# Kernel optimization log

Hardware: AMD Instinct MI355X
Metric: run time of the kernel (lower is better)

Reference implementation:

```python
import jax, jax.numpy as jnp
import numpy as np

N, D = 8192, 128
NOISEVAR = 1.0

def _softplusinverse(v):
    return np.log(1.0 - np.exp(-v)) + v

def setup_inputs() -> dict:
    key = jax.random.key(0)
    kx, kn = jax.random.split(key)
    x = jax.random.normal(kx, (N, D), dtype=jnp.float32)
    noise = jax.random.normal(kn, (N, D), dtype=jnp.float32)
    phi = jnp.asarray(_softplusinverse(NOISEVAR), dtype=jnp.float32)
    return {"x": x, "phi": phi, "noise": noise}

def reference(x, phi, noise):
    # x: [n, d] encoded features; phi: scalar noise param; noise: [n, d] i.i.d. N(0,1)
    n = x.shape[0]
    var = jax.nn.softplus(phi)
    # Pairwise squared L2 distances via Gram-matrix trick (same math as
    # norm(x_i - x_j)^2, avoids the [n, n, d] broadcast intermediate).
    sq = jnp.sum(x * x, axis=1)                                  # [n]
    d2 = jnp.maximum(sq[:, None] + sq[None, :] - 2.0 * (x @ x.T), 0.0)  # [n, n]
    kde_contribution = jnp.mean(jax.nn.logsumexp(-0.5 * d2 / var, axis=1))
    IXT_nats = jnp.log(jnp.float32(n)) - kde_contribution
    IXT = IXT_nats / jnp.log(jnp.float32(2.0))  # bits=True -> nats2bits
    out = x + var * noise                        # training=True noise injection
    return out, IXT
```

## Files before the change

### kernel.cpp

```cpp
#include <hip/hip_runtime.h>
#include <hip/hip_bf16.h>

#define N 8192
#define D 128
#define TILE 128
#define NT (N / TILE)

typedef __attribute__((ext_vector_type(8))) short short8;
typedef __attribute__((ext_vector_type(4))) float floatx4;
typedef unsigned int u32;

#define GLOAD_LDS16(g, l) \
    __builtin_amdgcn_global_load_lds((const __attribute__((address_space(1))) u32*)(g), \
                                     (__attribute__((address_space(3))) u32*)(l), 16, 0, 0)

static __device__ inline float softplus_of(const float* __restrict__ phi) {
    float p = phi[0];
    return (p > 20.f) ? p : log1pf(__expf(p));
}

static __device__ inline unsigned short f2bf(float f) {
    return __builtin_bit_cast(unsigned short, __float2bfloat16(f));
}

static __device__ inline short8 pack8(float4 a, float4 b) {
    short8 r;
    r[0] = (short)f2bf(a.x); r[1] = (short)f2bf(a.y);
    r[2] = (short)f2bf(a.z); r[3] = (short)f2bf(a.w);
    r[4] = (short)f2bf(b.x); r[5] = (short)f2bf(b.y);
    r[6] = (short)f2bf(b.z); r[7] = (short)f2bf(b.w);
    return r;
}

__global__ __launch_bounds__(256) void k1_cvt(
        const float* __restrict__ x, unsigned short* __restrict__ bf16x,
        float* __restrict__ sq, float* __restrict__ rowsum) {
    int gid = blockIdx.x * 256 + threadIdx.x;
    int row = gid >> 4;
    int gc  = gid & 15;
    const float* src = x + (size_t)row * D + gc * 8;
    float4 u = *(const float4*)src;
    float4 v = *(const float4*)(src + 4);
    short8 p = pack8(u, v);
    int gp = gc ^ (row & 15);
    *(short8*)&bf16x[(size_t)row * D + gp * 8] = p;

    float s = 0.f;
    #pragma unroll
    for (int k = 0; k < 8; k++) {
        u32 bits = ((u32)(unsigned short)p[k]) << 16;
        float b = __builtin_bit_cast(float, bits);
        s += b * b;
    }
    #pragma unroll
    for (int m = 1; m < 16; m <<= 1) s += __shfl_xor(s, m, 64);
    if (gc == 0) { sq[row] = s; rowsum[row] = 0.f; }
}

__global__ __launch_bounds__(256, 2) void k2_gram(
        const unsigned short* __restrict__ bf16x, const float* __restrict__ phi,
        const float* __restrict__ sq, float* __restrict__ rowsum) {
    __shared__ __align__(16) unsigned short Bs[2][TILE * D];

    const int t = threadIdx.x;
    const int wave = t >> 6;
    const int lane = t & 63;
    const int lrow = lane & 15;
    const int quad = lane >> 4;
    const int wr = (wave & 1) * 64;
    const int wc = (wave >> 1) * 64;

    const int b = blockIdx.x;
    const int cnt   = (b < 32) ? 5 : 4;
    const int start = (b < 32) ? 5 * b : 160 + 4 * (b - 32);

    int pti = 0, rem = start, len = NT;
    while (rem >= len) { rem -= len; ++pti; --len; }
    int ptj = pti + rem;

    float var = softplus_of(phi);
    const float e2c = (-0.5f / var) * 1.4426950408889634f;
    const float m2c = -2.0f * e2c;

    {
        const unsigned short* src = bf16x + (size_t)ptj * TILE * D;
        #pragma unroll
        for (int s = 0; s < 8; s++) {
            int cb = s * 256 + wave * 64;
            GLOAD_LDS16(src + (size_t)(cb + lane) * 8, &Bs[0][cb * 8]);
        }
    }
    __syncthreads();

    short8 af[4][4];
    float sie[4][4];
    float rowAcc[4][4];
    int curTi = -1;

    auto flushRow = [&]() {
        const int iBase = curTi * TILE;
        #pragma unroll
        for (int mt = 0; mt < 4; mt++)
            #pragma unroll
            for (int reg = 0; reg < 4; reg++) {
                float v = rowAcc[mt][reg];
                #pragma unroll
                for (int m = 1; m < 16; m <<= 1) v += __shfl_xor(v, m, 64);
                if (lrow == 0)
                    atomicAdd(&rowsum[iBase + wr + mt * 16 + quad * 4 + reg], v);
            }
    };

    for (int r = 0; r < cnt; ++r) {
        const int jBase = ptj * TILE;

        float sje[4];
        #pragma unroll
        for (int nt = 0; nt < 4; nt++)
            sje[nt] = sq[jBase + wc + nt * 16 + lrow] * e2c;

        int nti = pti, ntj = ptj + 1;
        if (ntj == NT) { ++nti; ntj = nti; }
        if (r + 1 < cnt) {
            const unsigned short* src = bf16x + (size_t)ntj * TILE * D;
            unsigned short* dstb = Bs[(r + 1) & 1];
            #pragma unroll
            for (int s = 0; s < 8; s++) {
                int cb = s * 256 + wave * 64;
                GLOAD_LDS16(src + (size_t)(cb + lane) * 8, &dstb[cb * 8]);
            }
        }

        if (pti != curTi) {
            if (curTi >= 0) flushRow();
            const int iBase = pti * TILE;
            #pragma unroll
            for (int mt = 0; mt < 4; mt++) {
                const unsigned short* arow =
                    bf16x + (size_t)(iBase + wr + mt * 16 + lrow) * D;
                #pragma unroll
                for (int kk = 0; kk < 4; kk++)
                    af[mt][kk] = *(const short8*)&arow[((kk * 4 + quad) ^ lrow) * 8];
            }
            #pragma unroll
            for (int mt = 0; mt < 4; mt++)
                #pragma unroll
                for (int reg = 0; reg < 4; reg++) {
                    sie[mt][reg] = sq[iBase + wr + mt * 16 + quad * 4 + reg] * e2c;
                    rowAcc[mt][reg] = 0.f;
                }
            curTi = pti;
        }

        const unsigned short* B = Bs[r & 1];
        floatx4 acc[4][4] = {};
        #pragma unroll
        for (int kk = 0; kk < 4; kk++) {
            short8 bfr[4];
            #pragma unroll
            for (int nt = 0; nt < 4; nt++) {
                int R = wc + nt * 16 + lrow;
                bfr[nt] = *(const short8*)&B[(size_t)R * D + ((kk * 4 + quad) ^ lrow) * 8];
            }
            #pragma unroll
            for (int mt = 0; mt < 4; mt++)
                #pragma unroll
                for (int nt = 0; nt < 4; nt++)
                    acc[mt][nt] = __builtin_amdgcn_mfma_f32_16x16x32_bf16(
                        af[mt][kk], bfr[nt], acc[mt][nt], 0, 0, 0);
        }

        float colAcc[4] = {0.f, 0.f, 0.f, 0.f};
        #pragma unroll
        for (int mt = 0; mt < 4; mt++) {
            #pragma unroll
            for (int reg = 0; reg < 4; reg++) {
                float base = sie[mt][reg];
                #pragma unroll
                for (int nt = 0; nt < 4; nt++) {
                    float p2 = fminf(fmaf(acc[mt][nt][reg], m2c, base + sje[nt]), 0.f);
                    float p = exp2f(p2);
                    rowAcc[mt][reg] += p;
                    colAcc[nt] += p;
                }
            }
        }

        if (pti != ptj) {
            #pragma unroll
            for (int nt = 0; nt < 4; nt++) {
                float v = colAcc[nt];
                v += __shfl_xor(v, 16, 64);
                v += __shfl_xor(v, 32, 64);
                if (quad == 0)
                    atomicAdd(&rowsum[jBase + wc + nt * 16 + lrow], v);
            }
        }

        pti = nti; ptj = ntj;
        __syncthreads();
    }

    flushRow();
}

__global__ __launch_bounds__(1024) void k3_final(
        const float* __restrict__ rowsum, float* __restrict__ out_ixt) {
    __shared__ float red[16];
    int t = threadIdx.x;
    float local = 0.f;
    for (int i = t; i < N; i += 1024) local += logf(rowsum[i]);
    #pragma unroll
    for (int m = 1; m < 64; m <<= 1) local += __shfl_xor(local, m, 64);
    if ((t & 63) == 0) red[t >> 6] = local;
    __syncthreads();
    if (t < 16) {
        float v = red[t];
        #pragma unroll
        for (int m = 1; m < 16; m <<= 1) v += __shfl_xor(v, m, 64);
        if (t == 0) {
            float kde = v / (float)N;
            out_ixt[0] = (logf((float)N) - kde) * 1.4426950408889634f;
        }
    }
}

__global__ __launch_bounds__(256) void k4_noise(
        const float4* __restrict__ x, const float* __restrict__ phi,
        const float4* __restrict__ noise, float4* __restrict__ out) {
    int i = blockIdx.x * 256 + threadIdx.x;
    float var = softplus_of(phi);
    float4 xv = x[i], nv = noise[i];
    float4 ov;
    ov.x = xv.x + var * nv.x;
    ov.y = xv.y + var * nv.y;
    ov.z = xv.z + var * nv.z;
    ov.w = xv.w + var * nv.w;
    out[i] = ov;
}

extern "C" void kernel_launch(void* const* d_in, const int* in_sizes, int n_in,
                              void* d_out, int out_size, void* d_ws, size_t ws_size,
                              hipStream_t stream) {
    const float* x     = (const float*)d_in[0];
    const float* phi   = (const float*)d_in[1];
    const float* noise = (const float*)d_in[2];
    float* out = (float*)d_out;

    float* rowsum = (float*)d_ws;
    float* sq     = rowsum + N;
    unsigned short* bf16x = (unsigned short*)d_out;

    k1_cvt<<<(N * 16) / 256, 256, 0, stream>>>(x, bf16x, sq, rowsum);
    k2_gram<<<512, 256, 0, stream>>>(bf16x, phi, sq, rowsum);
    k3_final<<<1, 1024, 0, stream>>>(rowsum, out + (size_t)N * D);
    k4_noise<<<(N * D / 4) / 256, 256, 0, stream>>>(
        (const float4*)x, phi, (const float4*)noise, (float4*)out);
}
```

Measured before the change: 97.11 us.

## Use per-wave 64x64 tiles with register-resident B and fuse noise output into prep

The Gram kernel now gives each wave its own 64x64 tile pair in the upper-triangular schedule. B fragments are loaded straight from global memory into registers and prefetched for the next tile, replacing the shared-memory double buffer and block-wide barriers. The noise-injection kernel is folded into the conversion kernel, and the bf16 copy moves to workspace so that kernel can write the output directly. This removes LDS traffic, syncs and one launch, but each wave now reloads its B tile from global/L2 with no sharing across the block, and more atomics are issued per output row.

```diff
diff --git a/kernel.cpp b/kernel.cpp
--- a/kernel.cpp
+++ b/kernel.cpp
@@ -3,16 +3,13 @@
 
 #define N 8192
 #define D 128
-#define TILE 128
-#define NT (N / TILE)
+#define T64 64
+#define NT64 (N / T64)
+#define NPAIR (NT64 * (NT64 + 1) / 2)
 
 typedef __attribute__((ext_vector_type(8))) short short8;
 typedef __attribute__((ext_vector_type(4))) float floatx4;
 typedef unsigned int u32;
-
-#define GLOAD_LDS16(g, l) \
-    __builtin_amdgcn_global_load_lds((const __attribute__((address_space(1))) u32*)(g), \
-                                     (__attribute__((address_space(3))) u32*)(l), 16, 0, 0)
 
 static __device__ inline float softplus_of(const float* __restrict__ phi) {
     float p = phi[0];
@@ -32,18 +29,31 @@
     return r;
 }
 
-__global__ __launch_bounds__(256) void k1_cvt(
-        const float* __restrict__ x, unsigned short* __restrict__ bf16x,
-        float* __restrict__ sq, float* __restrict__ rowsum) {
+__global__ __launch_bounds__(256) void k1_prep(
+        const float* __restrict__ x, const float* __restrict__ phi,
+        const float* __restrict__ noise, float* __restrict__ out,
+        unsigned short* __restrict__ bf16x, float* __restrict__ sq,
+        float* __restrict__ rowsum) {
     int gid = blockIdx.x * 256 + threadIdx.x;
     int row = gid >> 4;
     int gc  = gid & 15;
-    const float* src = x + (size_t)row * D + gc * 8;
-    float4 u = *(const float4*)src;
-    float4 v = *(const float4*)(src + 4);
+    float var = softplus_of(phi);
+
+    const float* xs = x     + (size_t)row * D + gc * 8;
+    const float* ns = noise + (size_t)row * D + gc * 8;
+    float4 u  = *(const float4*)xs, v  = *(const float4*)(xs + 4);
+    float4 nu = *(const float4*)ns, nv = *(const float4*)(ns + 4);
+
+    float4 o0, o1;
+    o0.x = u.x + var * nu.x; o0.y = u.y + var * nu.y;
+    o0.z = u.z + var * nu.z; o0.w = u.w + var * nu.w;
+    o1.x = v.x + var * nv.x; o1.y = v.y + var * nv.y;
+    o1.z = v.z + var * nv.z; o1.w = v.w + var * nv.w;
+    float* od = out + (size_t)row * D + gc * 8;
+    *(float4*)od = o0; *(float4*)(od + 4) = o1;
+
     short8 p = pack8(u, v);
-    int gp = gc ^ (row & 15);
-    *(short8*)&bf16x[(size_t)row * D + gp * 8] = p;
+    *(short8*)&bf16x[(size_t)row * D + (size_t)(gc ^ (row & 15)) * 8] = p;
 
     float s = 0.f;
     #pragma unroll
@@ -60,148 +70,139 @@
 __global__ __launch_bounds__(256, 2) void k2_gram(
         const unsigned short* __restrict__ bf16x, const float* __restrict__ phi,
         const float* __restrict__ sq, float* __restrict__ rowsum) {
-    __shared__ __align__(16) unsigned short Bs[2][TILE * D];
-
-    const int t = threadIdx.x;
-    const int wave = t >> 6;
-    const int lane = t & 63;
+    const int w    = blockIdx.x * 4 + (threadIdx.x >> 6);
+    const int lane = threadIdx.x & 63;
     const int lrow = lane & 15;
     const int quad = lane >> 4;
-    const int wr = (wave & 1) * 64;
-    const int wc = (wave >> 1) * 64;
-
-    const int b = blockIdx.x;
-    const int cnt   = (b < 32) ? 5 : 4;
-    const int start = (b < 32) ? 5 * b : 160 + 4 * (b - 32);
-
-    int pti = 0, rem = start, len = NT;
-    while (rem >= len) { rem -= len; ++pti; --len; }
-    int ptj = pti + rem;
+
+    const int cnt = (w < 64) ? 5 : 4;
+    int start     = (w < 64) ? 5 * w : 4 * w + 64;
+    int ti = 0, rem = start, len = NT64;
+    while (rem >= len) { rem -= len; ++ti; --len; }
+    int tj = ti + rem;
 
     float var = softplus_of(phi);
     const float e2c = (-0.5f / var) * 1.4426950408889634f;
     const float m2c = -2.0f * e2c;
 
+    short8 af[4][4], bf[4][4];
+    float  sie[4][4], rowAcc[4][4];
+    int curTi = -1;
+
     {
-        const unsigned short* src = bf16x + (size_t)ptj * TILE * D;
-        #pragma unroll
-        for (int s = 0; s < 8; s++) {
-            int cb = s * 256 + wave * 64;
-            GLOAD_LDS16(src + (size_t)(cb + lane) * 8, &Bs[0][cb * 8]);
-        }
-    }
-    __syncthreads();
-
-    short8 af[4][4];
-    float sie[4][4];
-    float rowAcc[4][4];
-    int curTi = -1;
-
-    auto flushRow = [&]() {
-        const int iBase = curTi * TILE;
-        #pragma unroll
-        for (int mt = 0; mt < 4; mt++)
-            #pragma unroll
-            for (int reg = 0; reg < 4; reg++) {
-                float v = rowAcc[mt][reg];
-                #pragma unroll
-                for (int m = 1; m < 16; m <<= 1) v += __shfl_xor(v, m, 64);
-                if (lrow == 0)
-                    atomicAdd(&rowsum[iBase + wr + mt * 16 + quad * 4 + reg], v);
-            }
-    };
+        const unsigned short* bb = bf16x + (size_t)tj * T64 * D;
+        #pragma unroll
+        for (int nt = 0; nt < 4; nt++) {
+            const unsigned short* br = bb + (size_t)(nt * 16 + lrow) * D;
+            #pragma unroll
+            for (int kk = 0; kk < 4; kk++)
+                bf[nt][kk] = *(const short8*)&br[((kk * 4 + quad) ^ lrow) * 8];
+        }
+    }
 
     for (int r = 0; r < cnt; ++r) {
-        const int jBase = ptj * TILE;
+        const int iB = ti * T64, jB = tj * T64;
 
         float sje[4];
         #pragma unroll
         for (int nt = 0; nt < 4; nt++)
-            sje[nt] = sq[jBase + wc + nt * 16 + lrow] * e2c;
-
-        int nti = pti, ntj = ptj + 1;
-        if (ntj == NT) { ++nti; ntj = nti; }
-        if (r + 1 < cnt) {
-            const unsigned short* src = bf16x + (size_t)ntj * TILE * D;
-            unsigned short* dstb = Bs[(r + 1) & 1];
-            #pragma unroll
-            for (int s = 0; s < 8; s++) {
-                int cb = s * 256 + wave * 64;
-                GLOAD_LDS16(src + (size_t)(cb + lane) * 8, &dstb[cb * 8]);
-            }
-        }
-
-        if (pti != curTi) {
-            if (curTi >= 0) flushRow();
-            const int iBase = pti * TILE;
+            sje[nt] = sq[jB + nt * 16 + lrow] * e2c;
+
+        if (ti != curTi) {
+            if (curTi >= 0) {
+                const int pB = curTi * T64;
+                #pragma unroll
+                for (int mt = 0; mt < 4; mt++)
+                    #pragma unroll
+                    for (int reg = 0; reg < 4; reg++) {
+                        float vv = rowAcc[mt][reg];
+                        #pragma unroll
+                        for (int m = 1; m < 16; m <<= 1) vv += __shfl_xor(vv, m, 64);
+                        if (lrow == 0)
+                            atomicAdd(&rowsum[pB + mt * 16 + quad * 4 + reg], vv);
+                    }
+            }
             #pragma unroll
             for (int mt = 0; mt < 4; mt++) {
-                const unsigned short* arow =
-                    bf16x + (size_t)(iBase + wr + mt * 16 + lrow) * D;
+                const unsigned short* ar = bf16x + (size_t)(iB + mt * 16 + lrow) * D;
                 #pragma unroll
                 for (int kk = 0; kk < 4; kk++)
-                    af[mt][kk] = *(const short8*)&arow[((kk * 4 + quad) ^ lrow) * 8];
+                    af[mt][kk] = *(const short8*)&ar[((kk * 4 + quad) ^ lrow) * 8];
             }
             #pragma unroll
             for (int mt = 0; mt < 4; mt++)
                 #pragma unroll
                 for (int reg = 0; reg < 4; reg++) {
-                    sie[mt][reg] = sq[iBase + wr + mt * 16 + quad * 4 + reg] * e2c;
+                    sie[mt][reg] = sq[iB + mt * 16 + quad * 4 + reg] * e2c;
                     rowAcc[mt][reg] = 0.f;
                 }
-            curTi = pti;
-        }
-
-        const unsigned short* B = Bs[r & 1];
-        floatx4 acc[4][4] = {};
-        #pragma unroll
-        for (int kk = 0; kk < 4; kk++) {
-            short8 bfr[4];
+            curTi = ti;
+        }
+
+        int nti = ti, ntj = tj + 1;
+        if (ntj == NT64) { ++nti; ntj = nti; }
+
+        float colAcc[4] = {0.f, 0.f, 0.f, 0.f};
+        #pragma unroll
+        for (int nt = 0; nt < 4; nt++) {
+            floatx4 acc[4] = {};
+            #pragma unroll
+            for (int kk = 0; kk < 4; kk++)
+                #pragma unroll
+                for (int mt = 0; mt < 4; mt++)
+                    acc[mt] = __builtin_amdgcn_mfma_f32_16x16x32_bf16(
+                        af[mt][kk], bf[nt][kk], acc[mt], 0, 0, 0);
+
+            if (nt == 3 && r + 1 < cnt) {
+                const unsigned short* bb = bf16x + (size_t)ntj * T64 * D;
+                #pragma unroll
+                for (int n2 = 0; n2 < 4; n2++) {
+                    const unsigned short* br = bb + (size_t)(n2 * 16 + lrow) * D;
+                    #pragma unroll
+                    for (int kk = 0; kk < 4; kk++)
+                        bf[n2][kk] = *(const short8*)&br[((kk * 4 + quad) ^ lrow) * 8];
+                }
+            }
+
+            float sj = sje[nt];
+            #pragma unroll
+            for (int mt = 0; mt < 4; mt++)
+                #pragma unroll
+                for (int reg = 0; reg < 4; reg++) {
+                    float p2 = fminf(fmaf(acc[mt][reg], m2c, sie[mt][reg] + sj), 0.f);
+                    float p  = __builtin_amdgcn_exp2f(p2);
+                    rowAcc[mt][reg] += p;
+                    colAcc[nt]      += p;
+                }
+        }
+
+        if (ti != tj) {
             #pragma unroll
             for (int nt = 0; nt < 4; nt++) {
-                int R = wc + nt * 16 + lrow;
-                bfr[nt] = *(const short8*)&B[(size_t)R * D + ((kk * 4 + quad) ^ lrow) * 8];
-            }
-            #pragma unroll
-            for (int mt = 0; mt < 4; mt++)
-                #pragma unroll
-                for (int nt = 0; nt < 4; nt++)
-                    acc[mt][nt] = __builtin_amdgcn_mfma_f32_16x16x32_bf16(
-                        af[mt][kk], bfr[nt], acc[mt][nt], 0, 0, 0);
-        }
-
-        float colAcc[4] = {0.f, 0.f, 0.f, 0.f};
-        #pragma unroll
-        for (int mt = 0; mt < 4; mt++) {
+                float vv = colAcc[nt];
+                vv += __shfl_xor(vv, 16, 64);
+                vv += __shfl_xor(vv, 32, 64);
+                if (quad == 0)
+                    atomicAdd(&rowsum[jB + nt * 16 + lrow], vv);
+            }
+        }
+
+        ti = nti; tj = ntj;
+    }
+
+    {
+        const int pB = curTi * T64;
+        #pragma unroll
+        for (int mt = 0; mt < 4; mt++)
             #pragma unroll
             for (int reg = 0; reg < 4; reg++) {
-                float base = sie[mt][reg];
-                #pragma unroll
-                for (int nt = 0; nt < 4; nt++) {
-                    float p2 = fminf(fmaf(acc[mt][nt][reg], m2c, base + sje[nt]), 0.f);
-                    float p = exp2f(p2);
-                    rowAcc[mt][reg] += p;
-                    colAcc[nt] += p;
-                }
-            }
-        }
-
-        if (pti != ptj) {
-            #pragma unroll
-            for (int nt = 0; nt < 4; nt++) {
-                float v = colAcc[nt];
-                v += __shfl_xor(v, 16, 64);
-                v += __shfl_xor(v, 32, 64);
-                if (quad == 0)
-                    atomicAdd(&rowsum[jBase + wc + nt * 16 + lrow], v);
-            }
-        }
-
-        pti = nti; ptj = ntj;
-        __syncthreads();
-    }
-
-    flushRow();
+                float vv = rowAcc[mt][reg];
+                #pragma unroll
+                for (int m = 1; m < 16; m <<= 1) vv += __shfl_xor(vv, m, 64);
+                if (lrow == 0)
+                    atomicAdd(&rowsum[pB + mt * 16 + quad * 4 + reg], vv);
+            }
+    }
 }
 
 __global__ __launch_bounds__(1024) void k3_final(
@@ -225,20 +226,6 @@
     }
 }
 
-__global__ __launch_bounds__(256) void k4_noise(
-        const float4* __restrict__ x, const float* __restrict__ phi,
-        const float4* __restrict__ noise, float4* __restrict__ out) {
-    int i = blockIdx.x * 256 + threadIdx.x;
-    float var = softplus_of(phi);
-    float4 xv = x[i], nv = noise[i];
-    float4 ov;
-    ov.x = xv.x + var * nv.x;
-    ov.y = xv.y + var * nv.y;
-    ov.z = xv.z + var * nv.z;
-    ov.w = xv.w + var * nv.w;
-    out[i] = ov;
-}
-
 extern "C" void kernel_launch(void* const* d_in, const int* in_sizes, int n_in,
                               void* d_out, int out_size, void* d_ws, size_t ws_size,
                               hipStream_t stream) {
@@ -249,11 +236,9 @@
 
     float* rowsum = (float*)d_ws;
     float* sq     = rowsum + N;
-    unsigned short* bf16x = (unsigned short*)d_out;
-
-    k1_cvt<<<(N * 16) / 256, 256, 0, stream>>>(x, bf16x, sq, rowsum);
+    unsigned short* bf16x = (unsigned short*)(sq + N);
+
+    k1_prep<<<(N * 16) / 256, 256, 0, stream>>>(x, phi, noise, out, bf16x, sq, rowsum);
     k2_gram<<<512, 256, 0, stream>>>(bf16x, phi, sq, rowsum);
     k3_final<<<1, 1024, 0, stream>>>(rowsum, out + (size_t)N * D);
-    k4_noise<<<(N * D / 4) / 256, 256, 0, stream>>>(
-        (const float4*)x, phi, (const float4*)noise, (float4*)out);
-}
+}
```

After: 98.62 us. No clear change (+1.5%).
